# Optimization experiments

Hardware: AMD Instinct MI355X
Metric: run time of the kernel (lower is better)

Reference implementation:

```python
import jax, jax.numpy as jnp
import numpy as np

B = 262144
IN_FEATURES = 128
OUT_FEATURES = 128
NQ_IN = IN_FEATURES // 4
NQ_OUT = OUT_FEATURES // 4


def setup_inputs() -> dict:
    key = jax.random.key(0)
    kx, kw, kb = jax.random.split(key, 3)
    stdv = 1.0 / np.sqrt(IN_FEATURES).astype(np.float32)
    x = jax.random.normal(kx, (B, IN_FEATURES), dtype=jnp.float32)
    weight = jax.random.uniform(kw, (NQ_OUT, NQ_IN, 4), dtype=jnp.float32,
                                minval=-stdv, maxval=stdv)
    bias = jax.random.uniform(kb, (OUT_FEATURES,), dtype=jnp.float32,
                              minval=-stdv, maxval=stdv)
    return {"x": x, "weight": weight, "bias": bias}


def reference(x, weight, bias):
    b = x.shape[0]
    nq_in = weight.shape[1]
    # [B, nq_in, 4] quaternion components
    xq = x.reshape(b, nq_in, 4)
    xa, xi, xj, xk = xq[..., 0], xq[..., 1], xq[..., 2], xq[..., 3]
    wa, wi, wj, wk = weight[..., 0], weight[..., 1], weight[..., 2], weight[..., 3]
    # each term: [B, nq_in] @ [nq_in, nq_out] -> [B, nq_out]
    mm = lambda u, w: jnp.einsum('bn,on->bo', u, w)
    out_a = mm(xa, wa) - mm(xi, wi) - mm(xj, wj) - mm(xk, wk)
    out_i = mm(xa, wi) + mm(xi, wa) + mm(xj, wk) - mm(xk, wj)
    out_j = mm(xa, wj) - mm(xi, wk) + mm(xj, wa) + mm(xk, wi)
    out_k = mm(xa, wk) + mm(xi, wj) - mm(xj, wi) + mm(xk, wa)
    out = jnp.stack([out_a, out_i, out_j, out_k], axis=-1).reshape(b, -1)
    return out + bias
```

## Files before the change

### kernel.cpp

```cpp
#include <hip/hip_runtime.h>
#include <hip/hip_bf16.h>

typedef __bf16 bf16x8 __attribute__((ext_vector_type(8)));
typedef float  f32x4  __attribute__((ext_vector_type(4)));

#define BATCH       262144
#define NTILES      (BATCH / 16)
#define GEMM_BLOCKS 1024

__global__ __launch_bounds__(256) void prep_wfrag(const float* __restrict__ w,
                                                  ushort* __restrict__ wfrag) {
    int t = blockIdx.x * 256 + threadIdx.x;
    if (t >= 128 * 128) return;
    int j    = t & 7;
    int lane = (t >> 3) & 63;
    int kb   = (t >> 9) & 3;
    int nt   = t >> 11;
    int n = nt * 16 + (lane & 15);
    int k = kb * 32 + (lane >> 4) * 8 + j;
    int o  = n >> 2, c = n & 3;
    int nq = k >> 2, d = k & 3;
    const int   comp[4][4] = {{0,1,2,3},{1,0,3,2},{2,3,0,1},{3,2,1,0}};
    const float sgn [4][4] = {{ 1.f,-1.f,-1.f,-1.f},
                              { 1.f, 1.f, 1.f,-1.f},
                              { 1.f,-1.f, 1.f, 1.f},
                              { 1.f, 1.f,-1.f, 1.f}};
    float val = sgn[c][d] * w[o * 128 + nq * 4 + comp[c][d]];
    __bf16 bv = (__bf16)val;
    wfrag[t] = *reinterpret_cast<ushort*>(&bv);
}

__global__ __launch_bounds__(512, 8) void qgemm(const float* __restrict__ x,
                                                const ushort* __restrict__ wfrag,
                                                const float* __restrict__ bias,
                                                float* __restrict__ out) {
    __shared__ __align__(16) ushort wlds[16384];
    __shared__ __align__(16) float  sbias[128];

    int tid = threadIdx.x;
    {
        const int4* src = (const int4*)wfrag;
        int4*       dst = (int4*)wlds;
#pragma unroll
        for (int i = 0; i < 4; ++i) dst[tid + i * 512] = src[tid + i * 512];
    }
    if (tid < 128) sbias[tid] = bias[tid];

    int lane  = tid & 63;
    int wid   = tid >> 6;
    int row16 = lane & 15;
    int kgrp  = lane >> 4;

    __syncthreads();

    const bf16x8* blds = (const bf16x8*)wlds;
    int gwave = blockIdx.x * 8 + wid;

    for (int tile = gwave; tile < NTILES; tile += GEMM_BLOCKS * 8) {
        const float* xt = x + (size_t)tile * 16 * 128;
        const float4* xv = (const float4*)(xt + row16 * 128 + kgrp * 8);
        bf16x8 afr[4];
#pragma unroll
        for (int kb = 0; kb < 4; ++kb) {
            float4 p = xv[kb * 8 + 0];
            float4 q = xv[kb * 8 + 1];
            afr[kb][0] = (__bf16)p.x; afr[kb][1] = (__bf16)p.y;
            afr[kb][2] = (__bf16)p.z; afr[kb][3] = (__bf16)p.w;
            afr[kb][4] = (__bf16)q.x; afr[kb][5] = (__bf16)q.y;
            afr[kb][6] = (__bf16)q.z; afr[kb][7] = (__bf16)q.w;
        }

        asm volatile("" ::: "memory");

        float* op = out + (size_t)tile * 16 * 128 + row16 * 128 + kgrp * 4;
#pragma unroll
        for (int nt = 0; nt < 8; ++nt) {
            f32x4 acc = *(const f32x4*)&sbias[nt * 16 + kgrp * 4];
#pragma unroll
            for (int kb = 0; kb < 4; ++kb) {
                bf16x8 wfr = blds[(nt * 4 + kb) * 64 + lane];
                acc = __builtin_amdgcn_mfma_f32_16x16x32_bf16(wfr, afr[kb], acc, 0, 0, 0);
            }
            __builtin_nontemporal_store(*(f32x4*)&acc, (f32x4*)(op + nt * 16));
        }
    }
}

extern "C" void kernel_launch(void* const* d_in, const int* in_sizes, int n_in,
                              void* d_out, int out_size, void* d_ws, size_t ws_size,
                              hipStream_t stream) {
    const float* x      = (const float*)d_in[0];
    const float* weight = (const float*)d_in[1];
    const float* bias   = (const float*)d_in[2];
    float*       out    = (float*)d_out;
    ushort*      wfrag  = (ushort*)d_ws;

    prep_wfrag<<<64, 256, 0, stream>>>(weight, wfrag);
    qgemm<<<GEMM_BLOCKS, 512, 0, stream>>>(x, wfrag, bias, out);
}
```

Measured before the change: 58.51 us.

## Fuse weight fragment construction into GEMM kernel and remap K ordering for x loads

Removes the separate prep kernel and has every GEMM block build its bf16 quaternion weight fragments in LDS straight from the fp32 weight, saving a launch and a workspace round trip. The K index permutation within each 32-wide block is changed so that lanes in a row group load float4s in an interleaved pattern, which should give better coalescing of x loads, and the weight permutation is adjusted to match. Output stores switch from nontemporal to regular stores. In exchange, every one of the 1024 blocks now redoes the scattered weight gather and sign computation.

```diff
diff --git a/kernel.cpp b/kernel.cpp
--- a/kernel.cpp
+++ b/kernel.cpp
@@ -8,41 +8,36 @@
 #define NTILES      (BATCH / 16)
 #define GEMM_BLOCKS 1024
 
-__global__ __launch_bounds__(256) void prep_wfrag(const float* __restrict__ w,
-                                                  ushort* __restrict__ wfrag) {
-    int t = blockIdx.x * 256 + threadIdx.x;
-    if (t >= 128 * 128) return;
-    int j    = t & 7;
-    int lane = (t >> 3) & 63;
-    int kb   = (t >> 9) & 3;
-    int nt   = t >> 11;
-    int n = nt * 16 + (lane & 15);
-    int k = kb * 32 + (lane >> 4) * 8 + j;
-    int o  = n >> 2, c = n & 3;
-    int nq = k >> 2, d = k & 3;
-    const int   comp[4][4] = {{0,1,2,3},{1,0,3,2},{2,3,0,1},{3,2,1,0}};
-    const float sgn [4][4] = {{ 1.f,-1.f,-1.f,-1.f},
-                              { 1.f, 1.f, 1.f,-1.f},
-                              { 1.f,-1.f, 1.f, 1.f},
-                              { 1.f, 1.f,-1.f, 1.f}};
-    float val = sgn[c][d] * w[o * 128 + nq * 4 + comp[c][d]];
-    __bf16 bv = (__bf16)val;
-    wfrag[t] = *reinterpret_cast<ushort*>(&bv);
-}
-
 __global__ __launch_bounds__(512, 8) void qgemm(const float* __restrict__ x,
-                                                const ushort* __restrict__ wfrag,
+                                                const float* __restrict__ w,
                                                 const float* __restrict__ bias,
                                                 float* __restrict__ out) {
     __shared__ __align__(16) ushort wlds[16384];
     __shared__ __align__(16) float  sbias[128];
 
     int tid = threadIdx.x;
-    {
-        const int4* src = (const int4*)wfrag;
-        int4*       dst = (int4*)wlds;
+
 #pragma unroll
-        for (int i = 0; i < 4; ++i) dst[tid + i * 512] = src[tid + i * 512];
+    for (int i = 0; i < 4; ++i) {
+        int f    = tid + i * 512;
+        int lane = f & 63;
+        int kb   = (f >> 6) & 3;
+        int nt   = f >> 8;
+        int g    = lane >> 4;
+        int n    = nt * 16 + (lane & 15);
+        int o = n >> 2, c = n & 3;
+        bf16x8 bv;
+#pragma unroll
+        for (int j = 0; j < 8; ++j) {
+            int k  = kb * 32 + (j < 4 ? g * 4 + j : 16 + g * 4 + (j - 4));
+            int nq = k >> 2, d = k & 3;
+            int comp = c ^ d;
+            bool neg = (d != 0) && ((c == 0) || (c != d && d != (c % 3) + 1));
+            float val = w[o * 128 + nq * 4 + comp];
+            val = neg ? -val : val;
+            bv[j] = (__bf16)val;
+        }
+        *reinterpret_cast<bf16x8*>(&wlds[f * 8]) = bv;
     }
     if (tid < 128) sbias[tid] = bias[tid];
 
@@ -57,13 +52,12 @@
     int gwave = blockIdx.x * 8 + wid;
 
     for (int tile = gwave; tile < NTILES; tile += GEMM_BLOCKS * 8) {
-        const float* xt = x + (size_t)tile * 16 * 128;
-        const float4* xv = (const float4*)(xt + row16 * 128 + kgrp * 8);
+        const float4* xv = (const float4*)(x + (size_t)tile * 16 * 128 + row16 * 128);
         bf16x8 afr[4];
 #pragma unroll
         for (int kb = 0; kb < 4; ++kb) {
-            float4 p = xv[kb * 8 + 0];
-            float4 q = xv[kb * 8 + 1];
+            float4 p = xv[kb * 8 + kgrp];
+            float4 q = xv[kb * 8 + kgrp + 4];
             afr[kb][0] = (__bf16)p.x; afr[kb][1] = (__bf16)p.y;
             afr[kb][2] = (__bf16)p.z; afr[kb][3] = (__bf16)p.w;
             afr[kb][4] = (__bf16)q.x; afr[kb][5] = (__bf16)q.y;
@@ -81,7 +75,7 @@
                 bf16x8 wfr = blds[(nt * 4 + kb) * 64 + lane];
                 acc = __builtin_amdgcn_mfma_f32_16x16x32_bf16(wfr, afr[kb], acc, 0, 0, 0);
             }
-            __builtin_nontemporal_store(*(f32x4*)&acc, (f32x4*)(op + nt * 16));
+            *(f32x4*)(op + nt * 16) = acc;
         }
     }
 }
@@ -93,8 +87,6 @@
     const float* weight = (const float*)d_in[1];
     const float* bias   = (const float*)d_in[2];
     float*       out    = (float*)d_out;
-    ushort*      wfrag  = (ushort*)d_ws;
 
-    prep_wfrag<<<64, 256, 0, stream>>>(weight, wfrag);
-    qgemm<<<GEMM_BLOCKS, 512, 0, stream>>>(x, wfrag, bias, out);
+    qgemm<<<GEMM_BLOCKS, 512, 0, stream>>>(x, weight, bias, out);
 }
```

After: 56.60 us. -3.3%, faster.

## Prefetch both tiles per wave up front with coalesced interleaved K layout

Applied to the files above, without the earlier changes.

Each wave now handles exactly two tiles and issues all x loads for both before any compute, so more loads are in flight at once. The K permutation in the weight fragments is changed so each lane group reads contiguous 16-byte chunks across kgrp, which gives more coalesced x loads. Nontemporal stores become plain stores, launch bounds drop to 4 waves/SIMD to allow more registers, and the sign/component table is replaced with bit logic. The loop is hardcoded to two tiles per wave, which relies on the fixed batch and grid size.

```diff
diff --git a/kernel.cpp b/kernel.cpp
--- a/kernel.cpp
+++ b/kernel.cpp
@@ -16,21 +16,20 @@
     int lane = (t >> 3) & 63;
     int kb   = (t >> 9) & 3;
     int nt   = t >> 11;
+    int g    = lane >> 4;
     int n = nt * 16 + (lane & 15);
-    int k = kb * 32 + (lane >> 4) * 8 + j;
+    int k = kb * 32 + (j < 4 ? g * 4 + j : 16 + g * 4 + (j - 4));
     int o  = n >> 2, c = n & 3;
     int nq = k >> 2, d = k & 3;
-    const int   comp[4][4] = {{0,1,2,3},{1,0,3,2},{2,3,0,1},{3,2,1,0}};
-    const float sgn [4][4] = {{ 1.f,-1.f,-1.f,-1.f},
-                              { 1.f, 1.f, 1.f,-1.f},
-                              { 1.f,-1.f, 1.f, 1.f},
-                              { 1.f, 1.f,-1.f, 1.f}};
-    float val = sgn[c][d] * w[o * 128 + nq * 4 + comp[c][d]];
+    int comp = c ^ d;
+    bool neg = (d != 0) && ((c == 0) || (c != d && d != (c % 3) + 1));
+    float val = w[o * 128 + nq * 4 + comp];
+    val = neg ? -val : val;
     __bf16 bv = (__bf16)val;
     wfrag[t] = *reinterpret_cast<ushort*>(&bv);
 }
 
-__global__ __launch_bounds__(512, 8) void qgemm(const float* __restrict__ x,
+__global__ __launch_bounds__(512, 4) void qgemm(const float* __restrict__ x,
                                                 const ushort* __restrict__ wfrag,
                                                 const float* __restrict__ bias,
                                                 float* __restrict__ out) {
@@ -55,24 +54,34 @@
 
     const bf16x8* blds = (const bf16x8*)wlds;
     int gwave = blockIdx.x * 8 + wid;
+    size_t t0 = (size_t)gwave;
+    size_t t1 = (size_t)gwave + 8192;
 
-    for (int tile = gwave; tile < NTILES; tile += GEMM_BLOCKS * 8) {
-        const float* xt = x + (size_t)tile * 16 * 128;
-        const float4* xv = (const float4*)(xt + row16 * 128 + kgrp * 8);
+    const float4* xv0 = (const float4*)(x + t0 * 2048 + row16 * 128);
+    const float4* xv1 = (const float4*)(x + t1 * 2048 + row16 * 128);
+    float4 r0[8], r1[8];
+#pragma unroll
+    for (int kb = 0; kb < 4; ++kb) {
+        r0[2 * kb]     = xv0[kb * 8 + kgrp];
+        r0[2 * kb + 1] = xv0[kb * 8 + kgrp + 4];
+    }
+#pragma unroll
+    for (int kb = 0; kb < 4; ++kb) {
+        r1[2 * kb]     = xv1[kb * 8 + kgrp];
+        r1[2 * kb + 1] = xv1[kb * 8 + kgrp + 4];
+    }
+
+    auto run_tile = [&](const float4* r, size_t tile) {
         bf16x8 afr[4];
 #pragma unroll
         for (int kb = 0; kb < 4; ++kb) {
-            float4 p = xv[kb * 8 + 0];
-            float4 q = xv[kb * 8 + 1];
+            float4 p = r[2 * kb], q = r[2 * kb + 1];
             afr[kb][0] = (__bf16)p.x; afr[kb][1] = (__bf16)p.y;
             afr[kb][2] = (__bf16)p.z; afr[kb][3] = (__bf16)p.w;
             afr[kb][4] = (__bf16)q.x; afr[kb][5] = (__bf16)q.y;
             afr[kb][6] = (__bf16)q.z; afr[kb][7] = (__bf16)q.w;
         }
-
-        asm volatile("" ::: "memory");
-
-        float* op = out + (size_t)tile * 16 * 128 + row16 * 128 + kgrp * 4;
+        float* op = out + tile * 2048 + row16 * 128 + kgrp * 4;
 #pragma unroll
         for (int nt = 0; nt < 8; ++nt) {
             f32x4 acc = *(const f32x4*)&sbias[nt * 16 + kgrp * 4];
@@ -81,9 +90,13 @@
                 bf16x8 wfr = blds[(nt * 4 + kb) * 64 + lane];
                 acc = __builtin_amdgcn_mfma_f32_16x16x32_bf16(wfr, afr[kb], acc, 0, 0, 0);
             }
-            __builtin_nontemporal_store(*(f32x4*)&acc, (f32x4*)(op + nt * 16));
+            *(f32x4*)(op + nt * 16) = acc;
         }
-    }
+    };
+
+    run_tile(r0, t0);
+    asm volatile("" ::: "memory");
+    run_tile(r1, t1);
 }
 
 extern "C" void kernel_launch(void* const* d_in, const int* in_sizes, int n_in,
```

Result: faster. 54.14 us (-7.5%).
